# Kernel optimization log

Measured on AMD Instinct MI355X. Metric: run time of the kernel, lower is better.

## Reference

```python
import jax, jax.numpy as jnp
import numpy as np

HIDDEN = 1024
MOE_FF = 512
SHARED_FF = 2816
NUM_EXPERTS = 16
TOP_K = 2
NORM_TOPK = True


def setup_inputs() -> dict:
    key = jax.random.key(0)
    ks = jax.random.split(key, 8)
    s = 0.02
    return {
        "layer_input": jax.random.normal(ks[0], (1, 2048, HIDDEN), dtype=jnp.float32),
        "gate_w": jax.random.normal(ks[1], (NUM_EXPERTS, HIDDEN), dtype=jnp.float32) * s,
        # fused gate_up weight per expert, laid out for x @ W: [E, hidden, 2*moe_ff]
        "w_gate_up": jax.random.normal(ks[2], (NUM_EXPERTS, HIDDEN, 2 * MOE_FF), dtype=jnp.float32) * s,
        # down weight per expert, laid out for h @ W: [E, moe_ff, hidden]
        "w_down": jax.random.normal(ks[3], (NUM_EXPERTS, MOE_FF, HIDDEN), dtype=jnp.float32) * s,
        # shared expert (Qwen2MoeMLP): Linear weights stored torch-style [out, in]
        "shared_w_gate": jax.random.normal(ks[4], (SHARED_FF, HIDDEN), dtype=jnp.float32) * s,
        "shared_w_up": jax.random.normal(ks[5], (SHARED_FF, HIDDEN), dtype=jnp.float32) * s,
        "shared_w_down": jax.random.normal(ks[6], (HIDDEN, SHARED_FF), dtype=jnp.float32) * s,
        "shared_gate_w": jax.random.normal(ks[7], (1, HIDDEN), dtype=jnp.float32) * s,
    }


def reference(layer_input, gate_w, w_gate_up, w_down,
              shared_w_gate, shared_w_up, shared_w_down, shared_gate_w):
    B, S, D = layer_input.shape
    x = layer_input.reshape(-1, D)  # [N, D]
    N = x.shape[0]

    # shared expert: silu-gated MLP, scaled by per-token sigmoid gate
    shared = (jax.nn.silu(x @ shared_w_gate.T) * (x @ shared_w_up.T)) @ shared_w_down.T
    shared = shared * jax.nn.sigmoid(x @ shared_gate_w.T)  # [N, D]

    # router: softmax in float32, top-k, optional renorm
    logits = x @ gate_w.T  # [N, E]
    probs = jax.nn.softmax(logits.astype(jnp.float32), axis=-1)
    rw, sel = jax.lax.top_k(probs, TOP_K)  # [N, K]
    if NORM_TOPK:
        rw = rw / rw.sum(axis=-1, keepdims=True)
    rw = rw.astype(x.dtype)

    # dense combine weights: zero for unselected experts (equivalent to
    # the sort/dispatch + grouped-GEMM + weighted scatter-combine)
    combine = jnp.zeros((N, NUM_EXPERTS), x.dtype).at[jnp.arange(N)[:, None], sel].set(rw)

    # expert gate_up projection, SwiGLU, down projection, weighted combine
    gu = jnp.einsum('nd,edf->nef', x, w_gate_up)  # [N, E, 2*moe_ff]
    g, h = jnp.split(gu, 2, axis=-1)
    h = jax.nn.silu(g) * h  # [N, E, moe_ff]
    expert_out = jnp.einsum('nef,efd,ne->nd', h, w_down, combine)  # [N, D]

    out = expert_out + shared
    return out.reshape(B, S, D)
```

## Files before the change

kernel.cpp:

```cpp
#include <hip/hip_runtime.h>
#include <hip/hip_bf16.h>

typedef unsigned short ushort_t;
typedef __bf16 bf16x8 __attribute__((ext_vector_type(8)));
typedef float f32x4 __attribute__((ext_vector_type(4)));

#define N_TOK 2048
#define DH    1024
#define FF    512
#define SFF   2816
#define NE    16

#define BM 128
#define BN 64
#define BK 64
#define LDK 72

__device__ __forceinline__ ushort_t f2bf(float f) {
  unsigned int x = __float_as_uint(f);
  unsigned int lsb = (x >> 16) & 1u;
  x += 0x7fffu + lsb;
  return (ushort_t)(x >> 16);
}

__device__ __forceinline__ uint4 cvt8v(const float4 a, const float4 b) {
  union { ushort_t u[8]; uint4 v; } r;
  r.u[0] = f2bf(a.x); r.u[1] = f2bf(a.y); r.u[2] = f2bf(a.z); r.u[3] = f2bf(a.w);
  r.u[4] = f2bf(b.x); r.u[5] = f2bf(b.y); r.u[6] = f2bf(b.z); r.u[7] = f2bf(b.w);
  return r.v;
}

__device__ __forceinline__ uint4 ld_cvt8(const float* __restrict__ p) {
  float4 a = *(const float4*)p;
  float4 b = *(const float4*)(p + 4);
  return cvt8v(a, b);
}

__global__ void out_epilogue_kernel(const float4* __restrict__ acc, float4* __restrict__ out) {
  size_t i = (size_t)blockIdx.x * 256 + threadIdx.x;
  out[i] = acc[i];
}

__global__ void router_kernel(const float* __restrict__ X, const float* __restrict__ GW,
                              const float* __restrict__ SGW,
                              int* __restrict__ sel, float* __restrict__ wtk,
                              float* __restrict__ sgate, float4* __restrict__ accv) {
  {
    size_t b0 = (size_t)blockIdx.x * 1024 + threadIdx.x;
    float4 z = make_float4(0.f, 0.f, 0.f, 0.f);
    accv[b0] = z; accv[b0 + 256] = z; accv[b0 + 512] = z; accv[b0 + 768] = z;
  }
  int wave = threadIdx.x >> 6, lane = threadIdx.x & 63;
  int n = blockIdx.x * 4 + wave;
  const float* x = X + (size_t)n * DH;
  int e = lane & 15, s = lane >> 4;
  const float* gw = GW + (size_t)e * DH;
  float lg = 0.f;
  for (int i = 0; i < 256; ++i) {
    int d = s * 256 + i;
    lg += x[d] * gw[d];
  }
  lg += __shfl_down(lg, 32);
  lg += __shfl_down(lg, 16);

  float gd = 0.f;
  #pragma unroll
  for (int i = 0; i < 16; ++i) {
    int d = lane * 16 + i;
    gd += x[d] * SGW[d];
  }
  #pragma unroll
  for (int off = 32; off >= 1; off >>= 1) gd += __shfl_down(gd, off);

  float l[16];
  #pragma unroll
  for (int i = 0; i < 16; ++i) l[i] = __shfl(lg, i);

  if (lane == 0) {
    int i1 = 0; float v1 = l[0];
    #pragma unroll
    for (int i = 1; i < 16; ++i) if (l[i] > v1) { v1 = l[i]; i1 = i; }
    int i2 = -1; float v2 = -1e30f;
    #pragma unroll
    for (int i = 0; i < 16; ++i) { if (i == i1) continue; if (l[i] > v2) { v2 = l[i]; i2 = i; } }
    float p2 = __expf(v2 - v1);
    float inv = 1.f / (1.f + p2);
    sel[n * 2 + 0] = i1; sel[n * 2 + 1] = i2;
    wtk[n * 2 + 0] = inv; wtk[n * 2 + 1] = p2 * inv;
    sgate[n] = 1.f / (1.f + __expf(-gd));
  }
}

__global__ void scatter_kernel(const int* __restrict__ sel, const float* __restrict__ wtk,
                               int* __restrict__ toks, float* __restrict__ wts,
                               int* __restrict__ offs) {
  __shared__ int cnt[NE], bas[NE];
  int t = threadIdx.x;
  if (t < NE) cnt[t] = 0;
  __syncthreads();
  for (int i = t; i < N_TOK * 2; i += 256) atomicAdd(&cnt[sel[i]], 1);
  __syncthreads();
  if (t == 0) {
    int s = 0;
    for (int e = 0; e < NE; ++e) { bas[e] = s; offs[e] = s; s += cnt[e]; }
    offs[NE] = s;
  }
  __syncthreads();
  if (t < NE) cnt[t] = 0;
  __syncthreads();
  for (int i = t; i < N_TOK * 2; i += 256) {
    int e = sel[i];
    int p = atomicAdd(&cnt[e], 1);
    int slot = bas[e] + p;
    toks[slot] = i >> 1;
    wts[slot]  = wtk[i];
  }
}

__global__ __launch_bounds__(256, 3) void gateup_kernel(
    const float* __restrict__ X, const float* __restrict__ WGU,
    const float* __restrict__ Bg, const float* __restrict__ Bu,
    ushort_t* __restrict__ HX, ushort_t* __restrict__ HS,
    const int* __restrict__ toks, const int* __restrict__ offs) {
  __shared__ __align__(16) ushort_t As[BM][LDK];
  __shared__ __align__(16) ushort_t Bgs[BN][LDK];
  __shared__ __align__(16) ushort_t Bus[BN][LDK];
  const int K = DH, NT = K / BK;

  int bid = blockIdx.x;
  int t = threadIdx.x;
  int wave = t >> 6, lane = t & 63;
  int wm = wave & 1, wn = wave >> 1;
  int qd = lane >> 4, l16 = lane & 15;
  int sr = t >> 3, sc = (t & 7) * 8;

  if (bid < 2048) {
    int e = bid >> 7, rem = bid & 127;
    int n0 = (rem & 7) * BN, m0 = (rem >> 3) * BM;
    int base = offs[e], M = offs[e + 1] - base;
    if (m0 >= M) return;
    const float* W = WGU + (size_t)e * DH * (2 * FF);
    int tn = t & 63, tk = (t >> 6) * 16;

    const float* arow[4];
    #pragma unroll
    for (int p = 0; p < 4; ++p) {
      int m = m0 + sr + 32 * p;
      int mm = m < M ? m : (M - 1);
      arow[p] = X + (size_t)toks[base + mm] * K + sc;
    }
    const float* wkb = W + (size_t)tk * (2 * FF) + n0 + tn;

    uint4 ar[4];
    float bgr[16], bur[16];
    #pragma unroll
    for (int p = 0; p < 4; ++p) ar[p] = ld_cvt8(arow[p]);
    #pragma unroll
    for (int j = 0; j < 16; ++j) {
      bgr[j] = wkb[(size_t)j * (2 * FF)];
      bur[j] = wkb[(size_t)j * (2 * FF) + FF];
    }

    f32x4 accg[4][2], accu[4][2];
    #pragma unroll
    for (int i = 0; i < 4; ++i)
      #pragma unroll
      for (int j = 0; j < 2; ++j) {
        accg[i][j] = (f32x4){0.f, 0.f, 0.f, 0.f};
        accu[i][j] = (f32x4){0.f, 0.f, 0.f, 0.f};
      }

    for (int kt = 0; kt < NT; ++kt) {
      #pragma unroll
      for (int p = 0; p < 4; ++p)
        *(uint4*)&As[sr + 32 * p][sc] = ar[p];
      {
        union { ushort_t u[8]; uint4 v; } g0, g1, u0, u1;
        #pragma unroll
        for (int j = 0; j < 8; ++j) {
          g0.u[j] = f2bf(bgr[j]); g1.u[j] = f2bf(bgr[8 + j]);
          u0.u[j] = f2bf(bur[j]); u1.u[j] = f2bf(bur[8 + j]);
        }
        *(uint4*)&Bgs[tn][tk]     = g0.v;
        *(uint4*)&Bgs[tn][tk + 8] = g1.v;
        *(uint4*)&Bus[tn][tk]     = u0.v;
        *(uint4*)&Bus[tn][tk + 8] = u1.v;
      }
      __syncthreads();
      if (kt + 1 < NT) {
        int ko = (kt + 1) * BK;
        #pragma unroll
        for (int p = 0; p < 4; ++p) ar[p] = ld_cvt8(arow[p] + ko);
        const float* wk = wkb + (size_t)ko * (2 * FF);
        #pragma unroll
        for (int j = 0; j < 16; ++j) {
          bgr[j] = wk[(size_t)j * (2 * FF)];
          bur[j] = wk[(size_t)j * (2 * FF) + FF];
        }
      }
      #pragma unroll
      for (int ks = 0; ks < 2; ++ks) {
        int kk = ks * 32 + qd * 8;
        bf16x8 af[4], bgf[2], buf[2];
        #pragma unroll
        for (int i = 0; i < 4; ++i)
          af[i] = *(const bf16x8*)&As[wm * 64 + i * 16 + l16][kk];
        #pragma unroll
        for (int j = 0; j < 2; ++j) {
          bgf[j] = *(const bf16x8*)&Bgs[wn * 32 + j * 16 + l16][kk];
          buf[j] = *(const bf16x8*)&Bus[wn * 32 + j * 16 + l16][kk];
        }
        #pragma unroll
        for (int i = 0; i < 4; ++i)
          #pragma unroll
          for (int j = 0; j < 2; ++j) {
            accg[i][j] = __builtin_amdgcn_mfma_f32_16x16x32_bf16(af[i], bgf[j], accg[i][j], 0, 0, 0);
            accu[i][j] = __builtin_amdgcn_mfma_f32_16x16x32_bf16(af[i], buf[j], accu[i][j], 0, 0, 0);
          }
      }
      __syncthreads();
    }

    #pragma unroll
    for (int i = 0; i < 4; ++i)
      #pragma unroll
      for (int r = 0; r < 4; ++r) {
        int m = m0 + wm * 64 + i * 16 + qd * 4 + r;
        if (m >= M) continue;
        #pragma unroll
        for (int j = 0; j < 2; ++j) {
          float g = accg[i][j][r], u = accu[i][j][r];
          float h = g / (1.f + __expf(-g)) * u;
          int col = n0 + wn * 32 + j * 16 + l16;
          HX[(size_t)(base + m) * FF + col] = f2bf(h);
        }
      }
  } else {
    unsigned s = bid - 2048;
    int n0 = (int)(s % 44u) * BN, m0 = (int)(s / 44u) * BM;

    const float* arow[4];
    const float *bgrow[2], *burow[2];
    #pragma unroll
    for (int p = 0; p < 4; ++p)
      arow[p] = X + (size_t)(m0 + sr + 32 * p) * K + sc;
    #pragma unroll
    for (int p = 0; p < 2; ++p) {
      bgrow[p] = Bg + (size_t)(n0 + sr + 32 * p) * K + sc;
      burow[p] = Bu + (size_t)(n0 + sr + 32 * p) * K + sc;
    }

    uint4 ar[4], bgr[2], bur[2];
    #pragma unroll
    for (int p = 0; p < 4; ++p) ar[p] = ld_cvt8(arow[p]);
    #pragma unroll
    for (int p = 0; p < 2; ++p) {
      bgr[p] = ld_cvt8(bgrow[p]);
      bur[p] = ld_cvt8(burow[p]);
    }

    f32x4 accg[4][2], accu[4][2];
    #pragma unroll
    for (int i = 0; i < 4; ++i)
      #pragma unroll
      for (int j = 0; j < 2; ++j) {
        accg[i][j] = (f32x4){0.f, 0.f, 0.f, 0.f};
        accu[i][j] = (f32x4){0.f, 0.f, 0.f, 0.f};
      }

    for (int kt = 0; kt < NT; ++kt) {
      #pragma unroll
      for (int p = 0; p < 4; ++p)
        *(uint4*)&As[sr + 32 * p][sc] = ar[p];
      #pragma unroll
      for (int p = 0; p < 2; ++p) {
        *(uint4*)&Bgs[sr + 32 * p][sc] = bgr[p];
        *(uint4*)&Bus[sr + 32 * p][sc] = bur[p];
      }
      __syncthreads();
      if (kt + 1 < NT) {
        int ko = (kt + 1) * BK;
        #pragma unroll
        for (int p = 0; p < 4; ++p) ar[p] = ld_cvt8(arow[p] + ko);
        #pragma unroll
        for (int p = 0; p < 2; ++p) {
          bgr[p] = ld_cvt8(bgrow[p] + ko);
          bur[p] = ld_cvt8(burow[p] + ko);
        }
      }
      #pragma unroll
      for (int ks = 0; ks < 2; ++ks) {
        int kk = ks * 32 + qd * 8;
        bf16x8 af[4], bgf[2], buf[2];
        #pragma unroll
        for (int i = 0; i < 4; ++i)
          af[i] = *(const bf16x8*)&As[wm * 64 + i * 16 + l16][kk];
        #pragma unroll
        for (int j = 0; j < 2; ++j) {
          bgf[j] = *(const bf16x8*)&Bgs[wn * 32 + j * 16 + l16][kk];
          buf[j] = *(const bf16x8*)&Bus[wn * 32 + j * 16 + l16][kk];
        }
        #pragma unroll
        for (int i = 0; i < 4; ++i)
          #pragma unroll
          for (int j = 0; j < 2; ++j) {
            accg[i][j] = __builtin_amdgcn_mfma_f32_16x16x32_bf16(af[i], bgf[j], accg[i][j], 0, 0, 0);
            accu[i][j] = __builtin_amdgcn_mfma_f32_16x16x32_bf16(af[i], buf[j], accu[i][j], 0, 0, 0);
          }
      }
      __syncthreads();
    }

    #pragma unroll
    for (int i = 0; i < 4; ++i)
      #pragma unroll
      for (int r = 0; r < 4; ++r) {
        int m = m0 + wm * 64 + i * 16 + qd * 4 + r;
        #pragma unroll
        for (int j = 0; j < 2; ++j) {
          float g = accg[i][j][r], u = accu[i][j][r];
          float h = g / (1.f + __expf(-g)) * u;
          int col = n0 + wn * 32 + j * 16 + l16;
          HS[(size_t)m * SFF + col] = f2bf(h);
        }
      }
  }
}

__global__ __launch_bounds__(256, 4) void down_kernel(
    const ushort_t* __restrict__ HX, const ushort_t* __restrict__ HS,
    const float* __restrict__ WDN, const float* __restrict__ SWD,
    float* __restrict__ acc, const int* __restrict__ toks,
    const float* __restrict__ wts, const int* __restrict__ offs,
    const float* __restrict__ sgate) {
  __shared__ __align__(16) ushort_t As[BM][LDK];
  __shared__ __align__(16) ushort_t Bs[BN][LDK];

  int bid = blockIdx.x;
  int t = threadIdx.x;
  int wave = t >> 6, lane = t & 63;
  int wm = wave & 1, wn = wave >> 1;
  int qd = lane >> 4, l16 = lane & 15;
  int sr = t >> 3, sc = (t & 7) * 8;

  if (bid < 4096) {
    int e = bid >> 8, rem = bid & 255;
    int n0 = (rem & 15) * BN, m0 = (rem >> 4) * BM;
    int base = offs[e], M = offs[e + 1] - base;
    if (m0 >= M) return;
    const int K = FF, NT = K / BK;
    const float* W = WDN + (size_t)e * FF * DH;
    const ushort_t* A = HX + (size_t)base * K;
    int tn = t & 63, tk = (t >> 6) * 16;

    const ushort_t* arow[4];
    #pragma unroll
    for (int p = 0; p < 4; ++p)
      arow[p] = A + (size_t)(m0 + sr + 32 * p) * K + sc;
    const float* wkb = W + (size_t)tk * DH + n0 + tn;

    uint4 ar[4];
    float br[16];
    #pragma unroll
    for (int p = 0; p < 4; ++p) ar[p] = *(const uint4*)(arow[p]);
    #pragma unroll
    for (int j = 0; j < 16; ++j) br[j] = wkb[(size_t)j * DH];

    f32x4 c[4][2];
    #pragma unroll
    for (int i = 0; i < 4; ++i)
      #pragma unroll
      for (int j = 0; j < 2; ++j) c[i][j] = (f32x4){0.f, 0.f, 0.f, 0.f};

    for (int kt = 0; kt < NT; ++kt) {
      #pragma unroll
      for (int p = 0; p < 4; ++p)
        *(uint4*)&As[sr + 32 * p][sc] = ar[p];
      {
        union { ushort_t u[8]; uint4 v; } b0, b1;
        #pragma unroll
        for (int j = 0; j < 8; ++j) { b0.u[j] = f2bf(br[j]); b1.u[j] = f2bf(br[8 + j]); }
        *(uint4*)&Bs[tn][tk]     = b0.v;
        *(uint4*)&Bs[tn][tk + 8] = b1.v;
      }
      __syncthreads();
      if (kt + 1 < NT) {
        int ko = (kt + 1) * BK;
        #pragma unroll
        for (int p = 0; p < 4; ++p) ar[p] = *(const uint4*)(arow[p] + ko);
        const float* wk = wkb + (size_t)ko * DH;
        #pragma unroll
        for (int j = 0; j < 16; ++j) br[j] = wk[(size_t)j * DH];
      }
      #pragma unroll
      for (int ks = 0; ks < 2; ++ks) {
        int kk = ks * 32 + qd * 8;
        bf16x8 af[4], bf[2];
        #pragma unroll
        for (int i = 0; i < 4; ++i)
          af[i] = *(const bf16x8*)&As[wm * 64 + i * 16 + l16][kk];
        #pragma unroll
        for (int j = 0; j < 2; ++j)
          bf[j] = *(const bf16x8*)&Bs[wn * 32 + j * 16 + l16][kk];
        #pragma unroll
        for (int i = 0; i < 4; ++i)
          #pragma unroll
          for (int j = 0; j < 2; ++j)
            c[i][j] = __builtin_amdgcn_mfma_f32_16x16x32_bf16(af[i], bf[j], c[i][j], 0, 0, 0);
      }
      __syncthreads();
    }

    #pragma unroll
    for (int i = 0; i < 4; ++i)
      #pragma unroll
      for (int r = 0; r < 4; ++r) {
        int m = m0 + wm * 64 + i * 16 + qd * 4 + r;
        if (m >= M) continue;
        int tok = toks[base + m];
        float w = wts[base + m];
        #pragma unroll
        for (int j = 0; j < 2; ++j) {
          int n = n0 + wn * 32 + j * 16 + l16;
          atomicAdd(&acc[(size_t)tok * DH + n], c[i][j][r] * w);
        }
      }
  } else {
    int s = bid - 4096;
    int kz = s >> 8, rem = s & 255;
    int n0 = (rem & 15) * BN, m0 = (rem >> 4) * BM;
    const int KC = SFF / 2, NT = KC / BK;
    int kb = kz * KC;

    const ushort_t* arow[4];
    const float* brow[2];
    #pragma unroll
    for (int p = 0; p < 4; ++p)
      arow[p] = HS + (size_t)(m0 + sr + 32 * p) * SFF + kb + sc;
    #pragma unroll
    for (int p = 0; p < 2; ++p)
      brow[p] = SWD + (size_t)(n0 + sr + 32 * p) * SFF + kb + sc;

    uint4 ar[4], br[2];
    #pragma unroll
    for (int p = 0; p < 4; ++p) ar[p] = *(const uint4*)(arow[p]);
    #pragma unroll
    for (int p = 0; p < 2; ++p) br[p] = ld_cvt8(brow[p]);

    f32x4 c[4][2];
    #pragma unroll
    for (int i = 0; i < 4; ++i)
      #pragma unroll
      for (int j = 0; j < 2; ++j) c[i][j] = (f32x4){0.f, 0.f, 0.f, 0.f};

    for (int kt = 0; kt < NT; ++kt) {
      #pragma unroll
      for (int p = 0; p < 4; ++p)
        *(uint4*)&As[sr + 32 * p][sc] = ar[p];
      #pragma unroll
      for (int p = 0; p < 2; ++p)
        *(uint4*)&Bs[sr + 32 * p][sc] = br[p];
      __syncthreads();
      if (kt + 1 < NT) {
        int ko = (kt + 1) * BK;
        #pragma unroll
        for (int p = 0; p < 4; ++p) ar[p] = *(const uint4*)(arow[p] + ko);
        #pragma unroll
        for (int p = 0; p < 2; ++p) br[p] = ld_cvt8(brow[p] + ko);
      }
      #pragma unroll
      for (int ks = 0; ks < 2; ++ks) {
        int kk = ks * 32 + qd * 8;
        bf16x8 af[4], bf[2];
        #pragma unroll
        for (int i = 0; i < 4; ++i)
          af[i] = *(const bf16x8*)&As[wm * 64 + i * 16 + l16][kk];
        #pragma unroll
        for (int j = 0; j < 2; ++j)
          bf[j] = *(const bf16x8*)&Bs[wn * 32 + j * 16 + l16][kk];
        #pragma unroll
        for (int i = 0; i < 4; ++i)
          #pragma unroll
          for (int j = 0; j < 2; ++j)
            c[i][j] = __builtin_amdgcn_mfma_f32_16x16x32_bf16(af[i], bf[j], c[i][j], 0, 0, 0);
      }
      __syncthreads();
    }

    #pragma unroll
    for (int i = 0; i < 4; ++i)
      #pragma unroll
      for (int r = 0; r < 4; ++r) {
        int m = m0 + wm * 64 + i * 16 + qd * 4 + r;
        float sg = sgate[m];
        #pragma unroll
        for (int j = 0; j < 2; ++j) {
          int n = n0 + wn * 32 + j * 16 + l16;
          atomicAdd(&acc[(size_t)m * DH + n], c[i][j][r] * sg);
        }
      }
  }
}

extern "C" void kernel_launch(void* const* d_in, const int* in_sizes, int n_in,
                              void* d_out, int out_size, void* d_ws, size_t ws_size,
                              hipStream_t stream) {
  const float* x    = (const float*)d_in[0];
  const float* gw   = (const float*)d_in[1];
  const float* wgu  = (const float*)d_in[2];
  const float* wdn  = (const float*)d_in[3];
  const float* swg  = (const float*)d_in[4];
  const float* swu  = (const float*)d_in[5];
  const float* swd  = (const float*)d_in[6];
  const float* sgw  = (const float*)d_in[7];
  float* out = (float*)d_out;

  char* ws = (char*)d_ws;
  constexpr size_t OFF_ACC  = 0;
  constexpr size_t OFF_HS   = OFF_ACC + (size_t)N_TOK * DH * 4;
  constexpr size_t OFF_HX   = OFF_HS  + (size_t)N_TOK * SFF * 2;
  constexpr size_t OFF_TOK  = OFF_HX  + (size_t)4224 * FF * 2;
  constexpr size_t OFF_WTS  = OFF_TOK + 4224 * 4;
  constexpr size_t OFF_OFFS = OFF_WTS + 4224 * 4;
  constexpr size_t OFF_SEL  = OFF_OFFS + 32 * 4;
  constexpr size_t OFF_WTK  = OFF_SEL + 4096 * 4;
  constexpr size_t OFF_SG   = OFF_WTK + 4096 * 4;

  float*    acc   = (float*)(ws + OFF_ACC);
  ushort_t* hs    = (ushort_t*)(ws + OFF_HS);
  ushort_t* hx    = (ushort_t*)(ws + OFF_HX);
  int*      toks  = (int*)(ws + OFF_TOK);
  float*    wts   = (float*)(ws + OFF_WTS);
  int*      offs  = (int*)(ws + OFF_OFFS);
  int*      sel   = (int*)(ws + OFF_SEL);
  float*    wtk   = (float*)(ws + OFF_WTK);
  float*    sgate = (float*)(ws + OFF_SG);

  router_kernel<<<N_TOK / 4, 256, 0, stream>>>(x, gw, sgw, sel, wtk, sgate, (float4*)acc);
  scatter_kernel<<<1, 256, 0, stream>>>(sel, wtk, toks, wts, offs);
  gateup_kernel<<<2048 + 704, 256, 0, stream>>>(x, wgu, swg, swu, hx, hs, toks, offs);
  down_kernel<<<4096 + 512, 256, 0, stream>>>(hx, hs, wdn, swd, acc, toks, wts, offs, sgate);
  out_epilogue_kernel<<<2048, 256, 0, stream>>>((const float4*)acc, (float4*)out);
}
```

Before: 436.7 us.

## Replace atomic scatter-add with bf16 partial outputs and gather-combine kernel

The down-projection no longer atomically adds fp32 results into a zeroed accumulator. Shared-expert split-K halves and per-slot expert outputs are now written as bf16 tiles, staged through LDS for coalesced 16-byte stores. A new combine kernel gathers each token's pieces and applies the sigmoid and routing weights, which removes the accumulator zeroing, the atomics and the copy epilogue. The gate-up kernel also reorders its blocks so shared-expert tiles launch first and stages its epilogue through LDS. In exchange, the partial sums are rounded to bf16 before the final combine, costing some precision, and an extra bf16 intermediate buffer is written and read back.

```diff
diff --git a/kernel.cpp b/kernel.cpp
--- a/kernel.cpp
+++ b/kernel.cpp
@@ -22,34 +22,25 @@
   x += 0x7fffu + lsb;
   return (ushort_t)(x >> 16);
 }
-
+__device__ __forceinline__ float bf2f(ushort_t u) {
+  union { unsigned int i; float f; } v; v.i = ((unsigned int)u) << 16; return v.f;
+}
 __device__ __forceinline__ uint4 cvt8v(const float4 a, const float4 b) {
   union { ushort_t u[8]; uint4 v; } r;
   r.u[0] = f2bf(a.x); r.u[1] = f2bf(a.y); r.u[2] = f2bf(a.z); r.u[3] = f2bf(a.w);
   r.u[4] = f2bf(b.x); r.u[5] = f2bf(b.y); r.u[6] = f2bf(b.z); r.u[7] = f2bf(b.w);
   return r.v;
 }
-
 __device__ __forceinline__ uint4 ld_cvt8(const float* __restrict__ p) {
   float4 a = *(const float4*)p;
   float4 b = *(const float4*)(p + 4);
   return cvt8v(a, b);
 }
 
-__global__ void out_epilogue_kernel(const float4* __restrict__ acc, float4* __restrict__ out) {
-  size_t i = (size_t)blockIdx.x * 256 + threadIdx.x;
-  out[i] = acc[i];
-}
-
 __global__ void router_kernel(const float* __restrict__ X, const float* __restrict__ GW,
                               const float* __restrict__ SGW,
                               int* __restrict__ sel, float* __restrict__ wtk,
-                              float* __restrict__ sgate, float4* __restrict__ accv) {
-  {
-    size_t b0 = (size_t)blockIdx.x * 1024 + threadIdx.x;
-    float4 z = make_float4(0.f, 0.f, 0.f, 0.f);
-    accv[b0] = z; accv[b0 + 256] = z; accv[b0 + 512] = z; accv[b0 + 768] = z;
-  }
+                              float* __restrict__ sgate) {
   int wave = threadIdx.x >> 6, lane = threadIdx.x & 63;
   int n = blockIdx.x * 4 + wave;
   const float* x = X + (size_t)n * DH;
@@ -91,8 +82,8 @@
   }
 }
 
-__global__ void scatter_kernel(const int* __restrict__ sel, const float* __restrict__ wtk,
-                               int* __restrict__ toks, float* __restrict__ wts,
+__global__ void scatter_kernel(const int* __restrict__ sel,
+                               int* __restrict__ toks, int* __restrict__ slot_of,
                                int* __restrict__ offs) {
   __shared__ int cnt[NE], bas[NE];
   int t = threadIdx.x;
@@ -113,13 +104,13 @@
     int p = atomicAdd(&cnt[e], 1);
     int slot = bas[e] + p;
     toks[slot] = i >> 1;
-    wts[slot]  = wtk[i];
+    slot_of[i] = slot;
   }
 }
 
 __global__ __launch_bounds__(256, 3) void gateup_kernel(
     const float* __restrict__ X, const float* __restrict__ WGU,
-    const float* __restrict__ Bg, const float* __restrict__ Bu,
+    const float* __restrict__ SWG, const float* __restrict__ SWU,
     ushort_t* __restrict__ HX, ushort_t* __restrict__ HS,
     const int* __restrict__ toks, const int* __restrict__ offs) {
   __shared__ __align__(16) ushort_t As[BM][LDK];
@@ -134,10 +125,81 @@
   int qd = lane >> 4, l16 = lane & 15;
   int sr = t >> 3, sc = (t & 7) * 8;
 
-  if (bid < 2048) {
-    int e = bid >> 7, rem = bid & 127;
-    int n0 = (rem & 7) * BN, m0 = (rem >> 3) * BM;
-    int base = offs[e], M = offs[e + 1] - base;
+  f32x4 accg[4][2], accu[4][2];
+  #pragma unroll
+  for (int i = 0; i < 4; ++i)
+    #pragma unroll
+    for (int j = 0; j < 2; ++j) {
+      accg[i][j] = (f32x4){0.f, 0.f, 0.f, 0.f};
+      accu[i][j] = (f32x4){0.f, 0.f, 0.f, 0.f};
+    }
+
+  int m0, n0, M, base, is_exp;
+
+  if (bid < 704) {
+    is_exp = 0; base = 0; M = N_TOK;
+    n0 = (bid % 44) * BN; m0 = (bid / 44) * BM;
+    const float* arow[4];
+    const float *bgrow[2], *burow[2];
+    #pragma unroll
+    for (int p = 0; p < 4; ++p)
+      arow[p] = X + (size_t)(m0 + sr + 32 * p) * K + sc;
+    #pragma unroll
+    for (int p = 0; p < 2; ++p) {
+      bgrow[p] = SWG + (size_t)(n0 + sr + 32 * p) * K + sc;
+      burow[p] = SWU + (size_t)(n0 + sr + 32 * p) * K + sc;
+    }
+    uint4 ar[4], bgr[2], bur[2];
+    #pragma unroll
+    for (int p = 0; p < 4; ++p) ar[p] = ld_cvt8(arow[p]);
+    #pragma unroll
+    for (int p = 0; p < 2; ++p) { bgr[p] = ld_cvt8(bgrow[p]); bur[p] = ld_cvt8(burow[p]); }
+
+    for (int kt = 0; kt < NT; ++kt) {
+      #pragma unroll
+      for (int p = 0; p < 4; ++p)
+        *(uint4*)&As[sr + 32 * p][sc] = ar[p];
+      #pragma unroll
+      for (int p = 0; p < 2; ++p) {
+        *(uint4*)&Bgs[sr + 32 * p][sc] = bgr[p];
+        *(uint4*)&Bus[sr + 32 * p][sc] = bur[p];
+      }
+      __syncthreads();
+      if (kt + 1 < NT) {
+        int ko = (kt + 1) * BK;
+        #pragma unroll
+        for (int p = 0; p < 4; ++p) ar[p] = ld_cvt8(arow[p] + ko);
+        #pragma unroll
+        for (int p = 0; p < 2; ++p) { bgr[p] = ld_cvt8(bgrow[p] + ko); bur[p] = ld_cvt8(burow[p] + ko); }
+      }
+      #pragma unroll
+      for (int ks = 0; ks < 2; ++ks) {
+        int kk = ks * 32 + qd * 8;
+        bf16x8 af[4], bgf[2], buf[2];
+        #pragma unroll
+        for (int i = 0; i < 4; ++i)
+          af[i] = *(const bf16x8*)&As[wm * 64 + i * 16 + l16][kk];
+        #pragma unroll
+        for (int j = 0; j < 2; ++j) {
+          bgf[j] = *(const bf16x8*)&Bgs[wn * 32 + j * 16 + l16][kk];
+          buf[j] = *(const bf16x8*)&Bus[wn * 32 + j * 16 + l16][kk];
+        }
+        #pragma unroll
+        for (int i = 0; i < 4; ++i)
+          #pragma unroll
+          for (int j = 0; j < 2; ++j) {
+            accg[i][j] = __builtin_amdgcn_mfma_f32_16x16x32_bf16(af[i], bgf[j], accg[i][j], 0, 0, 0);
+            accu[i][j] = __builtin_amdgcn_mfma_f32_16x16x32_bf16(af[i], buf[j], accu[i][j], 0, 0, 0);
+          }
+      }
+      __syncthreads();
+    }
+  } else {
+    is_exp = 1;
+    int b2 = bid - 704;
+    int e = b2 >> 7, rem = b2 & 127;
+    n0 = (rem & 7) * BN; m0 = (rem >> 3) * BM;
+    base = offs[e]; M = offs[e + 1] - base;
     if (m0 >= M) return;
     const float* W = WGU + (size_t)e * DH * (2 * FF);
     int tn = t & 63, tk = (t >> 6) * 16;
@@ -160,15 +222,6 @@
       bgr[j] = wkb[(size_t)j * (2 * FF)];
       bur[j] = wkb[(size_t)j * (2 * FF) + FF];
     }
-
-    f32x4 accg[4][2], accu[4][2];
-    #pragma unroll
-    for (int i = 0; i < 4; ++i)
-      #pragma unroll
-      for (int j = 0; j < 2; ++j) {
-        accg[i][j] = (f32x4){0.f, 0.f, 0.f, 0.f};
-        accu[i][j] = (f32x4){0.f, 0.f, 0.f, 0.f};
-      }
 
     for (int kt = 0; kt < NT; ++kt) {
       #pragma unroll
@@ -220,119 +273,42 @@
       }
       __syncthreads();
     }
-
-    #pragma unroll
-    for (int i = 0; i < 4; ++i)
-      #pragma unroll
-      for (int r = 0; r < 4; ++r) {
-        int m = m0 + wm * 64 + i * 16 + qd * 4 + r;
-        if (m >= M) continue;
-        #pragma unroll
-        for (int j = 0; j < 2; ++j) {
-          float g = accg[i][j][r], u = accu[i][j][r];
-          float h = g / (1.f + __expf(-g)) * u;
-          int col = n0 + wn * 32 + j * 16 + l16;
-          HX[(size_t)(base + m) * FF + col] = f2bf(h);
-        }
-      }
+  }
+
+  #pragma unroll
+  for (int i = 0; i < 4; ++i)
+    #pragma unroll
+    for (int r = 0; r < 4; ++r) {
+      int row = wm * 64 + i * 16 + qd * 4 + r;
+      #pragma unroll
+      for (int j = 0; j < 2; ++j) {
+        float g = accg[i][j][r], u = accu[i][j][r];
+        float h = g / (1.f + __expf(-g)) * u;
+        As[row][wn * 32 + j * 16 + l16] = f2bf(h);
+      }
+    }
+  __syncthreads();
+  if (is_exp) {
+    #pragma unroll
+    for (int p = 0; p < 4; ++p) {
+      int m = m0 + sr + 32 * p;
+      if (m < M)
+        *(uint4*)(HX + (size_t)(base + m) * FF + n0 + sc) = *(uint4*)&As[sr + 32 * p][sc];
+    }
   } else {
-    unsigned s = bid - 2048;
-    int n0 = (int)(s % 44u) * BN, m0 = (int)(s / 44u) * BM;
-
-    const float* arow[4];
-    const float *bgrow[2], *burow[2];
-    #pragma unroll
-    for (int p = 0; p < 4; ++p)
-      arow[p] = X + (size_t)(m0 + sr + 32 * p) * K + sc;
-    #pragma unroll
-    for (int p = 0; p < 2; ++p) {
-      bgrow[p] = Bg + (size_t)(n0 + sr + 32 * p) * K + sc;
-      burow[p] = Bu + (size_t)(n0 + sr + 32 * p) * K + sc;
-    }
-
-    uint4 ar[4], bgr[2], bur[2];
-    #pragma unroll
-    for (int p = 0; p < 4; ++p) ar[p] = ld_cvt8(arow[p]);
-    #pragma unroll
-    for (int p = 0; p < 2; ++p) {
-      bgr[p] = ld_cvt8(bgrow[p]);
-      bur[p] = ld_cvt8(burow[p]);
-    }
-
-    f32x4 accg[4][2], accu[4][2];
-    #pragma unroll
-    for (int i = 0; i < 4; ++i)
-      #pragma unroll
-      for (int j = 0; j < 2; ++j) {
-        accg[i][j] = (f32x4){0.f, 0.f, 0.f, 0.f};
-        accu[i][j] = (f32x4){0.f, 0.f, 0.f, 0.f};
-      }
-
-    for (int kt = 0; kt < NT; ++kt) {
-      #pragma unroll
-      for (int p = 0; p < 4; ++p)
-        *(uint4*)&As[sr + 32 * p][sc] = ar[p];
-      #pragma unroll
-      for (int p = 0; p < 2; ++p) {
-        *(uint4*)&Bgs[sr + 32 * p][sc] = bgr[p];
-        *(uint4*)&Bus[sr + 32 * p][sc] = bur[p];
-      }
-      __syncthreads();
-      if (kt + 1 < NT) {
-        int ko = (kt + 1) * BK;
-        #pragma unroll
-        for (int p = 0; p < 4; ++p) ar[p] = ld_cvt8(arow[p] + ko);
-        #pragma unroll
-        for (int p = 0; p < 2; ++p) {
-          bgr[p] = ld_cvt8(bgrow[p] + ko);
-          bur[p] = ld_cvt8(burow[p] + ko);
-        }
-      }
-      #pragma unroll
-      for (int ks = 0; ks < 2; ++ks) {
-        int kk = ks * 32 + qd * 8;
-        bf16x8 af[4], bgf[2], buf[2];
-        #pragma unroll
-        for (int i = 0; i < 4; ++i)
-          af[i] = *(const bf16x8*)&As[wm * 64 + i * 16 + l16][kk];
-        #pragma unroll
-        for (int j = 0; j < 2; ++j) {
-          bgf[j] = *(const bf16x8*)&Bgs[wn * 32 + j * 16 + l16][kk];
-          buf[j] = *(const bf16x8*)&Bus[wn * 32 + j * 16 + l16][kk];
-        }
-        #pragma unroll
-        for (int i = 0; i < 4; ++i)
-          #pragma unroll
-          for (int j = 0; j < 2; ++j) {
-            accg[i][j] = __builtin_amdgcn_mfma_f32_16x16x32_bf16(af[i], bgf[j], accg[i][j], 0, 0, 0);
-            accu[i][j] = __builtin_amdgcn_mfma_f32_16x16x32_bf16(af[i], buf[j], accu[i][j], 0, 0, 0);
-          }
-      }
-      __syncthreads();
-    }
-
-    #pragma unroll
-    for (int i = 0; i < 4; ++i)
-      #pragma unroll
-      for (int r = 0; r < 4; ++r) {
-        int m = m0 + wm * 64 + i * 16 + qd * 4 + r;
-        #pragma unroll
-        for (int j = 0; j < 2; ++j) {
-          float g = accg[i][j][r], u = accu[i][j][r];
-          float h = g / (1.f + __expf(-g)) * u;
-          int col = n0 + wn * 32 + j * 16 + l16;
-          HS[(size_t)m * SFF + col] = f2bf(h);
-        }
-      }
+    #pragma unroll
+    for (int p = 0; p < 4; ++p) {
+      int m = m0 + sr + 32 * p;
+      *(uint4*)(HS + (size_t)m * SFF + n0 + sc) = *(uint4*)&As[sr + 32 * p][sc];
+    }
   }
 }
 
 __global__ __launch_bounds__(256, 4) void down_kernel(
     const ushort_t* __restrict__ HX, const ushort_t* __restrict__ HS,
     const float* __restrict__ WDN, const float* __restrict__ SWD,
-    float* __restrict__ acc, const int* __restrict__ toks,
-    const float* __restrict__ wts, const int* __restrict__ offs,
-    const float* __restrict__ sgate) {
+    ushort_t* __restrict__ SD0, ushort_t* __restrict__ SD1,
+    ushort_t* __restrict__ EXPO, const int* __restrict__ offs) {
   __shared__ __align__(16) ushort_t As[BM][LDK];
   __shared__ __align__(16) ushort_t Bs[BN][LDK];
 
@@ -343,20 +319,92 @@
   int qd = lane >> 4, l16 = lane & 15;
   int sr = t >> 3, sc = (t & 7) * 8;
 
-  if (bid < 4096) {
-    int e = bid >> 8, rem = bid & 255;
-    int n0 = (rem & 15) * BN, m0 = (rem >> 4) * BM;
-    int base = offs[e], M = offs[e + 1] - base;
+  f32x4 c[4][2];
+  #pragma unroll
+  for (int i = 0; i < 4; ++i)
+    #pragma unroll
+    for (int j = 0; j < 2; ++j) c[i][j] = (f32x4){0.f, 0.f, 0.f, 0.f};
+
+  int m0, n0, M, base_row;
+  ushort_t* outp;
+
+  if (bid < 512) {
+    int kz = bid >> 8, rem = bid & 255;
+    m0 = (rem >> 4) * BM; n0 = (rem & 15) * BN;
+    M = N_TOK; base_row = 0;
+    const int KC = SFF / 2, NT = KC / BK;
+    int kb = kz * KC;
+    outp = kz ? SD1 : SD0;
+
+    const ushort_t* arow[4];
+    const float* brow[2];
+    #pragma unroll
+    for (int p = 0; p < 4; ++p)
+      arow[p] = HS + (size_t)(m0 + sr + 32 * p) * SFF + kb + sc;
+    #pragma unroll
+    for (int p = 0; p < 2; ++p)
+      brow[p] = SWD + (size_t)(n0 + sr + 32 * p) * SFF + kb + sc;
+
+    uint4 ar[4], br[2];
+    #pragma unroll
+    for (int p = 0; p < 4; ++p) ar[p] = *(const uint4*)(arow[p]);
+    #pragma unroll
+    for (int p = 0; p < 2; ++p) br[p] = ld_cvt8(brow[p]);
+
+    for (int kt = 0; kt < NT; ++kt) {
+      #pragma unroll
+      for (int p = 0; p < 4; ++p)
+        *(uint4*)&As[sr + 32 * p][sc] = ar[p];
+      #pragma unroll
+      for (int p = 0; p < 2; ++p)
+        *(uint4*)&Bs[sr + 32 * p][sc] = br[p];
+      __syncthreads();
+      if (kt + 1 < NT) {
+        int ko = (kt + 1) * BK;
+        #pragma unroll
+        for (int p = 0; p < 4; ++p) ar[p] = *(const uint4*)(arow[p] + ko);
+        #pragma unroll
+        for (int p = 0; p < 2; ++p) br[p] = ld_cvt8(brow[p] + ko);
+      }
+      #pragma unroll
+      for (int ks = 0; ks < 2; ++ks) {
+        int kk = ks * 32 + qd * 8;
+        bf16x8 af[4], bf[2];
+        #pragma unroll
+        for (int i = 0; i < 4; ++i)
+          af[i] = *(const bf16x8*)&As[wm * 64 + i * 16 + l16][kk];
+        #pragma unroll
+        for (int j = 0; j < 2; ++j)
+          bf[j] = *(const bf16x8*)&Bs[wn * 32 + j * 16 + l16][kk];
+        #pragma unroll
+        for (int i = 0; i < 4; ++i)
+          #pragma unroll
+          for (int j = 0; j < 2; ++j)
+            c[i][j] = __builtin_amdgcn_mfma_f32_16x16x32_bf16(af[i], bf[j], c[i][j], 0, 0, 0);
+      }
+      __syncthreads();
+    }
+  } else {
+    int b2 = bid - 512;
+    int e = b2 >> 8, rem = b2 & 255;
+    n0 = (rem & 15) * BN; m0 = (rem >> 4) * BM;
+    int base = offs[e];
+    M = offs[e + 1] - base;
     if (m0 >= M) return;
-    const int K = FF, NT = K / BK;
+    base_row = base;
+    const int NT = FF / BK;
     const float* W = WDN + (size_t)e * FF * DH;
-    const ushort_t* A = HX + (size_t)base * K;
+    const ushort_t* A = HX + (size_t)base * FF;
     int tn = t & 63, tk = (t >> 6) * 16;
+    outp = EXPO;
 
     const ushort_t* arow[4];
     #pragma unroll
-    for (int p = 0; p < 4; ++p)
-      arow[p] = A + (size_t)(m0 + sr + 32 * p) * K + sc;
+    for (int p = 0; p < 4; ++p) {
+      int m = m0 + sr + 32 * p;
+      int mm = m < M ? m : (M - 1);
+      arow[p] = A + (size_t)mm * FF + sc;
+    }
     const float* wkb = W + (size_t)tk * DH + n0 + tn;
 
     uint4 ar[4];
@@ -365,12 +413,6 @@
     for (int p = 0; p < 4; ++p) ar[p] = *(const uint4*)(arow[p]);
     #pragma unroll
     for (int j = 0; j < 16; ++j) br[j] = wkb[(size_t)j * DH];
-
-    f32x4 c[4][2];
-    #pragma unroll
-    for (int i = 0; i < 4; ++i)
-      #pragma unroll
-      for (int j = 0; j < 2; ++j) c[i][j] = (f32x4){0.f, 0.f, 0.f, 0.f};
 
     for (int kt = 0; kt < NT; ++kt) {
       #pragma unroll
@@ -410,96 +452,45 @@
       }
       __syncthreads();
     }
-
-    #pragma unroll
-    for (int i = 0; i < 4; ++i)
-      #pragma unroll
-      for (int r = 0; r < 4; ++r) {
-        int m = m0 + wm * 64 + i * 16 + qd * 4 + r;
-        if (m >= M) continue;
-        int tok = toks[base + m];
-        float w = wts[base + m];
-        #pragma unroll
-        for (int j = 0; j < 2; ++j) {
-          int n = n0 + wn * 32 + j * 16 + l16;
-          atomicAdd(&acc[(size_t)tok * DH + n], c[i][j][r] * w);
-        }
-      }
-  } else {
-    int s = bid - 4096;
-    int kz = s >> 8, rem = s & 255;
-    int n0 = (rem & 15) * BN, m0 = (rem >> 4) * BM;
-    const int KC = SFF / 2, NT = KC / BK;
-    int kb = kz * KC;
-
-    const ushort_t* arow[4];
-    const float* brow[2];
-    #pragma unroll
-    for (int p = 0; p < 4; ++p)
-      arow[p] = HS + (size_t)(m0 + sr + 32 * p) * SFF + kb + sc;
-    #pragma unroll
-    for (int p = 0; p < 2; ++p)
-      brow[p] = SWD + (size_t)(n0 + sr + 32 * p) * SFF + kb + sc;
-
-    uint4 ar[4], br[2];
-    #pragma unroll
-    for (int p = 0; p < 4; ++p) ar[p] = *(const uint4*)(arow[p]);
-    #pragma unroll
-    for (int p = 0; p < 2; ++p) br[p] = ld_cvt8(brow[p]);
-
-    f32x4 c[4][2];
-    #pragma unroll
-    for (int i = 0; i < 4; ++i)
-      #pragma unroll
-      for (int j = 0; j < 2; ++j) c[i][j] = (f32x4){0.f, 0.f, 0.f, 0.f};
-
-    for (int kt = 0; kt < NT; ++kt) {
-      #pragma unroll
-      for (int p = 0; p < 4; ++p)
-        *(uint4*)&As[sr + 32 * p][sc] = ar[p];
-      #pragma unroll
-      for (int p = 0; p < 2; ++p)
-        *(uint4*)&Bs[sr + 32 * p][sc] = br[p];
-      __syncthreads();
-      if (kt + 1 < NT) {
-        int ko = (kt + 1) * BK;
-        #pragma unroll
-        for (int p = 0; p < 4; ++p) ar[p] = *(const uint4*)(arow[p] + ko);
-        #pragma unroll
-        for (int p = 0; p < 2; ++p) br[p] = ld_cvt8(brow[p] + ko);
-      }
-      #pragma unroll
-      for (int ks = 0; ks < 2; ++ks) {
-        int kk = ks * 32 + qd * 8;
-        bf16x8 af[4], bf[2];
-        #pragma unroll
-        for (int i = 0; i < 4; ++i)
-          af[i] = *(const bf16x8*)&As[wm * 64 + i * 16 + l16][kk];
-        #pragma unroll
-        for (int j = 0; j < 2; ++j)
-          bf[j] = *(const bf16x8*)&Bs[wn * 32 + j * 16 + l16][kk];
-        #pragma unroll
-        for (int i = 0; i < 4; ++i)
-          #pragma unroll
-          for (int j = 0; j < 2; ++j)
-            c[i][j] = __builtin_amdgcn_mfma_f32_16x16x32_bf16(af[i], bf[j], c[i][j], 0, 0, 0);
-      }
-      __syncthreads();
-    }
-
-    #pragma unroll
-    for (int i = 0; i < 4; ++i)
-      #pragma unroll
-      for (int r = 0; r < 4; ++r) {
-        int m = m0 + wm * 64 + i * 16 + qd * 4 + r;
-        float sg = sgate[m];
-        #pragma unroll
-        for (int j = 0; j < 2; ++j) {
-          int n = n0 + wn * 32 + j * 16 + l16;
-          atomicAdd(&acc[(size_t)m * DH + n], c[i][j][r] * sg);
-        }
-      }
-  }
+  }
+
+  #pragma unroll
+  for (int i = 0; i < 4; ++i)
+    #pragma unroll
+    for (int r = 0; r < 4; ++r) {
+      int row = wm * 64 + i * 16 + qd * 4 + r;
+      #pragma unroll
+      for (int j = 0; j < 2; ++j)
+        As[row][wn * 32 + j * 16 + l16] = f2bf(c[i][j][r]);
+    }
+  __syncthreads();
+  #pragma unroll
+  for (int p = 0; p < 4; ++p) {
+    int m = m0 + sr + 32 * p;
+    if (m < M)
+      *(uint4*)(outp + (size_t)(base_row + m) * DH + n0 + sc) = *(uint4*)&As[sr + 32 * p][sc];
+  }
+}
+
+__global__ void combine_kernel(const ushort_t* __restrict__ SD0, const ushort_t* __restrict__ SD1,
+                               const ushort_t* __restrict__ EXPO,
+                               const float* __restrict__ sgate, const float* __restrict__ wtk,
+                               const int* __restrict__ slot_of, float* __restrict__ out) {
+  int n = blockIdx.x, t = threadIdx.x;
+  float sg = sgate[n];
+  float w0 = wtk[n * 2 + 0], w1 = wtk[n * 2 + 1];
+  int s0 = slot_of[n * 2 + 0], s1 = slot_of[n * 2 + 1];
+  int col = t * 4;
+  ushort4 d0 = *(const ushort4*)(SD0 + (size_t)n * DH + col);
+  ushort4 d1 = *(const ushort4*)(SD1 + (size_t)n * DH + col);
+  ushort4 a  = *(const ushort4*)(EXPO + (size_t)s0 * DH + col);
+  ushort4 b  = *(const ushort4*)(EXPO + (size_t)s1 * DH + col);
+  float4 o;
+  o.x = sg * (bf2f(d0.x) + bf2f(d1.x)) + w0 * bf2f(a.x) + w1 * bf2f(b.x);
+  o.y = sg * (bf2f(d0.y) + bf2f(d1.y)) + w0 * bf2f(a.y) + w1 * bf2f(b.y);
+  o.z = sg * (bf2f(d0.z) + bf2f(d1.z)) + w0 * bf2f(a.z) + w1 * bf2f(b.z);
+  o.w = sg * (bf2f(d0.w) + bf2f(d1.w)) + w0 * bf2f(a.w) + w1 * bf2f(b.w);
+  *(float4*)(out + (size_t)n * DH + col) = o;
 }
 
 extern "C" void kernel_launch(void* const* d_in, const int* in_sizes, int n_in,
@@ -516,29 +507,33 @@
   float* out = (float*)d_out;
 
   char* ws = (char*)d_ws;
-  constexpr size_t OFF_ACC  = 0;
-  constexpr size_t OFF_HS   = OFF_ACC + (size_t)N_TOK * DH * 4;
-  constexpr size_t OFF_HX   = OFF_HS  + (size_t)N_TOK * SFF * 2;
-  constexpr size_t OFF_TOK  = OFF_HX  + (size_t)4224 * FF * 2;
-  constexpr size_t OFF_WTS  = OFF_TOK + 4224 * 4;
-  constexpr size_t OFF_OFFS = OFF_WTS + 4224 * 4;
+  constexpr size_t OFF_HS   = 0;
+  constexpr size_t OFF_HX   = OFF_HS   + (size_t)N_TOK * SFF * 2;
+  constexpr size_t OFF_SD0  = OFF_HX   + (size_t)4096 * FF * 2;
+  constexpr size_t OFF_SD1  = OFF_SD0  + (size_t)N_TOK * DH * 2;
+  constexpr size_t OFF_EXPO = OFF_SD1  + (size_t)N_TOK * DH * 2;
+  constexpr size_t OFF_TOK  = OFF_EXPO + (size_t)4096 * DH * 2;
+  constexpr size_t OFF_OFFS = OFF_TOK  + 4096 * 4;
   constexpr size_t OFF_SEL  = OFF_OFFS + 32 * 4;
-  constexpr size_t OFF_WTK  = OFF_SEL + 4096 * 4;
-  constexpr size_t OFF_SG   = OFF_WTK + 4096 * 4;
-
-  float*    acc   = (float*)(ws + OFF_ACC);
+  constexpr size_t OFF_WTK  = OFF_SEL  + 4096 * 4;
+  constexpr size_t OFF_SG   = OFF_WTK  + 4096 * 4;
+  constexpr size_t OFF_SLOT = OFF_SG   + 2048 * 4;
+
   ushort_t* hs    = (ushort_t*)(ws + OFF_HS);
   ushort_t* hx    = (ushort_t*)(ws + OFF_HX);
+  ushort_t* sd0   = (ushort_t*)(ws + OFF_SD0);
+  ushort_t* sd1   = (ushort_t*)(ws + OFF_SD1);
+  ushort_t* expo  = (ushort_t*)(ws + OFF_EXPO);
   int*      toks  = (int*)(ws + OFF_TOK);
-  float*    wts   = (float*)(ws + OFF_WTS);
   int*      offs  = (int*)(ws + OFF_OFFS);
   int*      sel   = (int*)(ws + OFF_SEL);
   float*    wtk   = (float*)(ws + OFF_WTK);
   float*    sgate = (float*)(ws + OFF_SG);
-
-  router_kernel<<<N_TOK / 4, 256, 0, stream>>>(x, gw, sgw, sel, wtk, sgate, (float4*)acc);
-  scatter_kernel<<<1, 256, 0, stream>>>(sel, wtk, toks, wts, offs);
-  gateup_kernel<<<2048 + 704, 256, 0, stream>>>(x, wgu, swg, swu, hx, hs, toks, offs);
-  down_kernel<<<4096 + 512, 256, 0, stream>>>(hx, hs, wdn, swd, acc, toks, wts, offs, sgate);
-  out_epilogue_kernel<<<2048, 256, 0, stream>>>((const float4*)acc, (float4*)out);
-}
+  int*      slot_of = (int*)(ws + OFF_SLOT);
+
+  router_kernel<<<N_TOK / 4, 256, 0, stream>>>(x, gw, sgw, sel, wtk, sgate);
+  scatter_kernel<<<1, 256, 0, stream>>>(sel, toks, slot_of, offs);
+  gateup_kernel<<<704 + 2048, 256, 0, stream>>>(x, wgu, swg, swu, hx, hs, toks, offs);
+  down_kernel<<<512 + 4096, 256, 0, stream>>>(hx, hs, wdn, swd, sd0, sd1, expo, offs);
+  combine_kernel<<<N_TOK, 256, 0, stream>>>(sd0, sd1, expo, sgate, wtk, slot_of, out);
+}
```

New measurement: 409.3 us. -6.3%, faster.
